# Optimization experiments

Hardware: AMD Instinct MI355X
Metric: run time of the kernel (lower is better)

## Reference

```python
import jax, jax.numpy as jnp
import numpy as np

IMG = 640
NUM_CLASSES = 80
B = 8
MAX_BOXES = 32
ALPHA, GAMMA = 0.25, 2.0
EPS = 1e-7


def make_anchors(img_size=IMG):
    strides = [8, 16, 32, 64, 128]
    scales = [2.0 ** 0, 2.0 ** (1.0 / 3.0), 2.0 ** (2.0 / 3.0)]
    ratios = [0.5, 1.0, 2.0]
    out = []
    for s in strides:
        base = 4.0 * s
        fs = img_size // s
        cs = (np.arange(fs) + 0.5) * s
        cy, cx = np.meshgrid(cs, cs, indexing='ij')
        for r in ratios:
            for sc in scales:
                w = base * sc / np.sqrt(r)
                h = base * sc * np.sqrt(r)
                a = np.stack([cx - w / 2, cy - h / 2, cx + w / 2, cy + h / 2], axis=-1).reshape(-1, 4)
                out.append(a)
    return np.concatenate(out, 0).astype(np.float32)  # [76725, 4]


def setup_inputs() -> dict:
    key = jax.random.key(0)
    k1, k2 = jax.random.split(key)
    anchors = jnp.asarray(make_anchors())
    Na = anchors.shape[0]
    cls_pred = jax.random.uniform(k1, (B, NUM_CLASSES, Na), dtype=jnp.float32)
    reg_pred = jax.random.normal(k2, (B, 4, Na), dtype=jnp.float32)
    rng = np.random.RandomState(0)
    x1 = rng.uniform(0, 500, (B, MAX_BOXES)).astype(np.float32)
    y1 = rng.uniform(0, 500, (B, MAX_BOXES)).astype(np.float32)
    w = rng.uniform(10, 140, (B, MAX_BOXES)).astype(np.float32)
    h = rng.uniform(10, 140, (B, MAX_BOXES)).astype(np.float32)
    cls = rng.randint(0, NUM_CLASSES, (B, MAX_BOXES)).astype(np.float32)
    nb = rng.randint(0, MAX_BOXES + 1, (B,))
    pad = np.arange(MAX_BOXES)[None, :] >= nb[:, None]
    cls[pad] = -1.0
    annots = jnp.asarray(np.stack([x1, y1, x1 + w, y1 + h, cls], axis=-1))  # [B,32,5]
    return {"cls_pred": cls_pred, "reg_pred": reg_pred, "annots": annots, "anchors": anchors}


def calc_iou(anchors, boxes):
    # anchors [Na,4], boxes [Nb,4] -> [Na,Nb]
    a_area = ((anchors[:, 2] - anchors[:, 0]) * (anchors[:, 3] - anchors[:, 1]))[:, None]
    b_area = (boxes[:, 2] - boxes[:, 0]) * (boxes[:, 3] - boxes[:, 1])
    iw = jnp.clip(jnp.minimum(anchors[:, 2:3], boxes[:, 2]) - jnp.maximum(anchors[:, 0:1], boxes[:, 0]), 0.0)
    ih = jnp.clip(jnp.minimum(anchors[:, 3:4], boxes[:, 3]) - jnp.maximum(anchors[:, 1:2], boxes[:, 1]), 0.0)
    inter = iw * ih
    union = jnp.clip(a_area + b_area - inter, 1e-7)
    return inter / union


def multibox_loss(cls_pred, reg_pred, annots, anchors):
    aw = anchors[:, 2] - anchors[:, 0]
    ah = anchors[:, 3] - anchors[:, 1]
    acx = anchors[:, 0] + 0.5 * aw
    acy = anchors[:, 1] + 0.5 * ah
    p = jnp.clip(cls_pred, EPS, 1.0 - EPS)
    C = cls_pred.shape[1]

    def per_image(classification, regression, annot):
        valid = annot[:, 4] != -1.0  # [Nb]
        iou = jnp.where(valid[None, :], calc_iou(anchors, annot[:, :4]), -1.0)  # [Na,Nb]
        iou_max = iou.max(axis=1)
        iou_arg = iou.argmax(axis=1)
        positive = iou_max >= 0.5  # [Na]
        num_pos = positive.sum().astype(jnp.float32)
        assigned = annot[iou_arg]  # [Na,5]
        tgt_cls = jnp.where(positive, assigned[:, 4].astype(jnp.int32), -1)
        targets = jax.nn.one_hot(tgt_cls, C, dtype=classification.dtype).T  # [C,Na]
        # focal loss (alpha=0.25, gamma=2) on clamped probabilities
        bce = -(targets * jnp.log(classification) + (1.0 - targets) * jnp.log1p(-classification))
        pt = targets * classification + (1.0 - targets) * (1.0 - classification)
        alpha_t = ALPHA * targets + (1.0 - ALPHA) * (1.0 - targets)
        cls_loss = (alpha_t * (1.0 - pt) ** GAMMA * bce).sum() / jnp.maximum(num_pos, 1.0)
        gw_raw = assigned[:, 2] - assigned[:, 0]
        gh_raw = assigned[:, 3] - assigned[:, 1]
        gcx = assigned[:, 0] + 0.5 * gw_raw
        gcy = assigned[:, 1] + 0.5 * gh_raw
        gw = jnp.clip(gw_raw, 1.0)
        gh = jnp.clip(gh_raw, 1.0)
        dx = (gcx - acx) / aw / 0.1
        dy = (gcy - acy) / ah / 0.1
        dw = jnp.log(gw / aw) / 0.2
        dh = jnp.log(gh / ah) / 0.2
        t = jnp.stack((dx, dy, dw, dh))  # [4,Na]
        diff = jnp.abs(t - regression)
        sl1 = jnp.where(diff <= 1.0 / 9.0, 0.5 * 9.0 * diff * diff, diff - 0.5 / 9.0)
        posf = positive.astype(regression.dtype)[None, :]
        reg_loss = jnp.where(num_pos > 0, (sl1 * posf).sum() / jnp.maximum(4.0 * num_pos, 1.0), 0.0)
        return cls_loss, reg_loss

    cls_l, reg_l = jax.vmap(per_image)(p, reg_pred, annots)
    return cls_l.mean() + reg_l.mean()


def reference(cls_pred, reg_pred, annots, anchors):
    return multibox_loss(cls_pred, reg_pred, annots, anchors)
```

## Files before the change

### kernel.cpp

```cpp
#include <hip/hip_runtime.h>
#include <math.h>


namespace {

constexpr int C  = 80;
constexpr int MB = 32;

__device__ __forceinline__ float clampp(float p) {
    return __builtin_amdgcn_fmed3f(p, 1e-7f, (float)(1.0 - 1e-7));
}

__global__ __launch_bounds__(256) void assign_kernel(
    const float* __restrict__ cls_pred,
    const float* __restrict__ reg_pred,
    const float* __restrict__ annots,
    const float* __restrict__ anchors,
    double* __restrict__ cls_sum,
    double* __restrict__ reg_sum,
    unsigned int* __restrict__ num_pos,
    int Na)
{
    const int b   = blockIdx.y;
    const int tid = threadIdx.x;
    const int a   = blockIdx.x * 256 + tid;
    const bool inb = (a < Na);

    __shared__ float4 sbox[MB];
    __shared__ float2 smeta[MB];
    __shared__ double swd[4];
    __shared__ float  swf[4];
    __shared__ int    swi[4];

    if (tid < MB) {
        const float* an = annots + ((size_t)b * MB + tid) * 5;
        float x1 = an[0], y1 = an[1], x2 = an[2], y2 = an[3];
        const float cl = an[4];
        if (cl == -1.0f) { x1 = y1 = x2 = y2 = -1e30f; }
        sbox[tid]  = make_float4(x1, y1, x2, y2);
        smeta[tid] = make_float2(__fmul_rn(__fsub_rn(x2, x1), __fsub_rn(y2, y1)), cl);
    }
    __syncthreads();

    float ax1 = 0.f, ay1 = 0.f, ax2 = 0.f, ay2 = 0.f;
    if (inb) {
        const float4 av = *reinterpret_cast<const float4*>(anchors + (size_t)a * 4);
        ax1 = av.x; ay1 = av.y; ax2 = av.z; ay2 = av.w;
    }
    const float a_area = __fmul_rn(__fsub_rn(ax2, ax1), __fsub_rn(ay2, ay1));

    float ibest = -1.0f, ubest = 1.0f;
    int   jbest = 0;
    #pragma unroll
    for (int j = 0; j < MB; ++j) {
        const float4 bx = sbox[j];
        const float2 bm = smeta[j];
        const float iw    = fmaxf(__fsub_rn(fminf(ax2, bx.z), fmaxf(ax1, bx.x)), 0.0f);
        const float ih    = fmaxf(__fsub_rn(fminf(ay2, bx.w), fmaxf(ay1, bx.y)), 0.0f);
        const float inter = __fmul_rn(iw, ih);
        const float uni   = fmaxf(__fsub_rn(__fadd_rn(a_area, bm.x), inter), 1e-7f);
        if (inter * ubest > ibest * uni) { ibest = inter; ubest = uni; jbest = j; }
    }

    double corr   = 0.0;
    float  my_reg = 0.0f;
    int    my_pos = 0;
    if (inb && __fdiv_rn(ibest, ubest) >= 0.5f) {
        my_pos = 1;
        const float4 g  = sbox[jbest];
        const int    tc = (int)smeta[jbest].y;

        const float aw  = ax2 - ax1,          ah  = ay2 - ay1;
        const float acx = ax1 + 0.5f * aw,    acy = ay1 + 0.5f * ah;
        const float gwr = g.z - g.x,          ghr = g.w - g.y;
        const float gcx = g.x + 0.5f * gwr,   gcy = g.y + 0.5f * ghr;
        const float gw  = fmaxf(gwr, 1.0f),   gh  = fmaxf(ghr, 1.0f);
        float t[4];
        t[0] = ((gcx - acx) / aw) / 0.1f;
        t[1] = ((gcy - acy) / ah) / 0.1f;
        t[2] = __logf(gw / aw) / 0.2f;
        t[3] = __logf(gh / ah) / 0.2f;
        const size_t rb = ((size_t)b * 4) * (size_t)Na + (size_t)a;
        #pragma unroll
        for (int k = 0; k < 4; ++k) {
            const float d = fabsf(t[k] - reg_pred[rb + (size_t)k * Na]);
            my_reg += (d <= (1.0f / 9.0f)) ? 4.5f * d * d : d - (0.5f / 9.0f);
        }

        float p = clampp(cls_pred[((size_t)b * C + tc) * (size_t)Na + (size_t)a]);
        const float om = __fsub_rn(1.0f, p);
        const float q  = __fsub_rn(1.0f, om);
        const float Ln = __logf(om);
        const float Lp = __logf(p);
        const float neg = -0.75f * __fmul_rn(__fmul_rn(q, q), Ln);
        const float pos = 0.25f * __fmul_rn(__fmul_rn(om, om), -Lp);
        corr = (double)pos - (double)neg;
    }

    double rc = corr;
    float  rr = my_reg;
    int    rp = my_pos;
    #pragma unroll
    for (int off = 32; off > 0; off >>= 1) {
        rc += __shfl_down(rc, off);
        rr += __shfl_down(rr, off);
        rp += __shfl_down(rp, off);
    }
    const int w = tid >> 6;
    if ((tid & 63) == 0) { swd[w] = rc; swf[w] = rr; swi[w] = rp; }
    __syncthreads();
    if (tid == 0) {
        double tcorr = 0.0; float treg = 0.f; int tpos = 0;
        #pragma unroll
        for (int i = 0; i < 4; ++i) { tcorr += swd[i]; treg += swf[i]; tpos += swi[i]; }
        if (tcorr != 0.0) atomicAdd(&cls_sum[b], tcorr);
        if (treg  != 0.f) atomicAdd(&reg_sum[b], (double)treg);
        if (tpos)         atomicAdd(&num_pos[b], (unsigned int)tpos);
    }
}

__global__ __launch_bounds__(256) void negsum_kernel(
    const float* __restrict__ cls_pred,
    double* __restrict__ cls_sum,
    int Na)
{
    const int b = blockIdx.y;
    const float4* __restrict__ base =
        reinterpret_cast<const float4*>(cls_pred + (size_t)b * C * (size_t)Na);
    const int n4     = (C * Na) >> 2;
    const int stride = gridDim.x * 256;

    float a0 = 0.f, a1 = 0.f, a2 = 0.f, a3 = 0.f;
    #pragma unroll 4
    for (int i = blockIdx.x * 256 + threadIdx.x; i < n4; i += stride) {
        const float4 v = base[i];
        {   const float p = clampp(v.x);
            const float om = __fsub_rn(1.0f, p);
            const float q  = __fsub_rn(1.0f, om);
            a0 = fmaf(__fmul_rn(__fmul_rn(q, q), __logf(om)), -0.75f, a0); }
        {   const float p = clampp(v.y);
            const float om = __fsub_rn(1.0f, p);
            const float q  = __fsub_rn(1.0f, om);
            a1 = fmaf(__fmul_rn(__fmul_rn(q, q), __logf(om)), -0.75f, a1); }
        {   const float p = clampp(v.z);
            const float om = __fsub_rn(1.0f, p);
            const float q  = __fsub_rn(1.0f, om);
            a2 = fmaf(__fmul_rn(__fmul_rn(q, q), __logf(om)), -0.75f, a2); }
        {   const float p = clampp(v.w);
            const float om = __fsub_rn(1.0f, p);
            const float q  = __fsub_rn(1.0f, om);
            a3 = fmaf(__fmul_rn(__fmul_rn(q, q), __logf(om)), -0.75f, a3); }
    }
    float csum = (a0 + a1) + (a2 + a3);

    #pragma unroll
    for (int off = 32; off > 0; off >>= 1) csum += __shfl_down(csum, off);
    __shared__ float sw[4];
    const int tid = threadIdx.x;
    const int w = tid >> 6;
    if ((tid & 63) == 0) sw[w] = csum;
    __syncthreads();
    if (tid == 0) {
        const float tot = (sw[0] + sw[1]) + (sw[2] + sw[3]);
        atomicAdd(&cls_sum[b], (double)tot);
    }
}

__global__ void finalize_kernel(const double* __restrict__ cls_sum,
                                const double* __restrict__ reg_sum,
                                const unsigned int* __restrict__ num_pos,
                                float* __restrict__ out, int B)
{
    if (threadIdx.x == 0 && blockIdx.x == 0) {
        double tot = 0.0;
        for (int b = 0; b < B; ++b) {
            const double np = (double)num_pos[b];
            tot += cls_sum[b] / fmax(np, 1.0);
            if (np > 0.0) tot += reg_sum[b] / (4.0 * np);
        }
        out[0] = (float)(tot / (double)B);
    }
}

}

extern "C" void kernel_launch(void* const* d_in, const int* in_sizes, int n_in,
                              void* d_out, int out_size, void* d_ws, size_t ws_size,
                              hipStream_t stream)
{
    const float* cls_pred = (const float*)d_in[0];
    const float* reg_pred = (const float*)d_in[1];
    const float* annots   = (const float*)d_in[2];
    const float* anchors  = (const float*)d_in[3];
    float* out = (float*)d_out;

    const int Na = in_sizes[3] / 4;
    const int B  = in_sizes[2] / (MB * 5);

    double*       cls_sum = (double*)d_ws;
    double*       reg_sum = cls_sum + B;
    unsigned int* num_pos = (unsigned int*)(reg_sum + B);

    hipMemsetAsync(d_ws, 0,
                   (size_t)(2 * B) * sizeof(double) + (size_t)B * sizeof(unsigned int),
                   stream);

    dim3 grid1((Na + 255) / 256, B);
    assign_kernel<<<grid1, 256, 0, stream>>>(cls_pred, reg_pred, annots, anchors,
                                             cls_sum, reg_sum, num_pos, Na);

    dim3 grid2(256, B);
    negsum_kernel<<<grid2, 256, 0, stream>>>(cls_pred, cls_sum, Na);

    finalize_kernel<<<1, 64, 0, stream>>>(cls_sum, reg_sum, num_pos, out, B);
}
```

Baseline: 294.0 us.

## Fuse assign and negative-sum kernels into one launch with per-block partials

Merges the anchor-assignment kernel and the negative focal-sum kernel into a single launch, split by block index range. Global double atomics and the workspace memset are replaced by per-block partial-sum buffers, which a 64-thread finalize kernel reduces with wave shuffles. This removes one kernel launch, the memset and atomic contention, and lets the two independent workloads run concurrently on the GPU. In exchange, the finalize kernel now reads more partial values, and block scheduling mixes two workloads with different costs.

```diff
diff --git a/kernel.cpp b/kernel.cpp
--- a/kernel.cpp
+++ b/kernel.cpp
@@ -4,33 +4,70 @@
 
 namespace {
 
-constexpr int C  = 80;
-constexpr int MB = 32;
+constexpr int C      = 80;
+constexpr int MB     = 32;
+constexpr int NB_NEG = 256;
 
 __device__ __forceinline__ float clampp(float p) {
     return __builtin_amdgcn_fmed3f(p, 1e-7f, (float)(1.0 - 1e-7));
 }
 
-__global__ __launch_bounds__(256) void assign_kernel(
+__device__ __forceinline__ float neg_term(float pin) {
+    const float p  = clampp(pin);
+    const float om = __fsub_rn(1.0f, p);
+    const float q  = __fsub_rn(1.0f, om);
+    return -0.75f * __fmul_rn(__fmul_rn(q, q), __logf(om));
+}
+
+__global__ __launch_bounds__(256) void main_kernel(
     const float* __restrict__ cls_pred,
     const float* __restrict__ reg_pred,
     const float* __restrict__ annots,
     const float* __restrict__ anchors,
-    double* __restrict__ cls_sum,
-    double* __restrict__ reg_sum,
-    unsigned int* __restrict__ num_pos,
-    int Na)
+    double* __restrict__ negPart,
+    double* __restrict__ corrPart,
+    float*  __restrict__ regPart,
+    int*    __restrict__ posPart,
+    int Na, int nbA)
 {
     const int b   = blockIdx.y;
     const int tid = threadIdx.x;
-    const int a   = blockIdx.x * 256 + tid;
-    const bool inb = (a < Na);
 
     __shared__ float4 sbox[MB];
     __shared__ float2 smeta[MB];
     __shared__ double swd[4];
     __shared__ float  swf[4];
     __shared__ int    swi[4];
+
+    if (blockIdx.x < NB_NEG) {
+        const float4* __restrict__ base =
+            reinterpret_cast<const float4*>(cls_pred + (size_t)b * C * (size_t)Na);
+        const int n4     = (C * Na) >> 2;
+        const int stride = NB_NEG * 256;
+
+        float a0 = 0.f, a1 = 0.f, a2 = 0.f, a3 = 0.f;
+        #pragma unroll 4
+        for (int i = blockIdx.x * 256 + tid; i < n4; i += stride) {
+            const float4 v = base[i];
+            a0 += neg_term(v.x);
+            a1 += neg_term(v.y);
+            a2 += neg_term(v.z);
+            a3 += neg_term(v.w);
+        }
+        float csum = (a0 + a1) + (a2 + a3);
+        #pragma unroll
+        for (int off = 32; off > 0; off >>= 1) csum += __shfl_down(csum, off);
+        if ((tid & 63) == 0) swf[tid >> 6] = csum;
+        __syncthreads();
+        if (tid == 0)
+            negPart[(size_t)b * NB_NEG + blockIdx.x] =
+                (double)((swf[0] + swf[1]) + (swf[2] + swf[3]));
+        return;
+    }
+
+    const int bx  = blockIdx.x - NB_NEG;
+    const int a   = bx * 256 + tid;
+    const bool inb = (a < Na);
 
     if (tid < MB) {
         const float* an = annots + ((size_t)b * MB + tid) * 5;
@@ -53,10 +90,10 @@
     int   jbest = 0;
     #pragma unroll
     for (int j = 0; j < MB; ++j) {
-        const float4 bx = sbox[j];
-        const float2 bm = smeta[j];
-        const float iw    = fmaxf(__fsub_rn(fminf(ax2, bx.z), fmaxf(ax1, bx.x)), 0.0f);
-        const float ih    = fmaxf(__fsub_rn(fminf(ay2, bx.w), fmaxf(ay1, bx.y)), 0.0f);
+        const float4 bxv = sbox[j];
+        const float2 bm  = smeta[j];
+        const float iw    = fmaxf(__fsub_rn(fminf(ax2, bxv.z), fmaxf(ax1, bxv.x)), 0.0f);
+        const float ih    = fmaxf(__fsub_rn(fminf(ay2, bxv.w), fmaxf(ay1, bxv.y)), 0.0f);
         const float inter = __fmul_rn(iw, ih);
         const float uni   = fmaxf(__fsub_rn(__fadd_rn(a_area, bm.x), inter), 1e-7f);
         if (inter * ubest > ibest * uni) { ibest = inter; ubest = uni; jbest = j; }
@@ -87,14 +124,10 @@
             my_reg += (d <= (1.0f / 9.0f)) ? 4.5f * d * d : d - (0.5f / 9.0f);
         }
 
-        float p = clampp(cls_pred[((size_t)b * C + tc) * (size_t)Na + (size_t)a]);
+        const float p  = clampp(cls_pred[((size_t)b * C + tc) * (size_t)Na + (size_t)a]);
         const float om = __fsub_rn(1.0f, p);
-        const float q  = __fsub_rn(1.0f, om);
-        const float Ln = __logf(om);
-        const float Lp = __logf(p);
-        const float neg = -0.75f * __fmul_rn(__fmul_rn(q, q), Ln);
-        const float pos = 0.25f * __fmul_rn(__fmul_rn(om, om), -Lp);
-        corr = (double)pos - (double)neg;
+        const float pos = 0.25f * __fmul_rn(__fmul_rn(om, om), -__logf(p));
+        corr = (double)pos - (double)neg_term(p);
     }
 
     double rc = corr;
@@ -113,73 +146,44 @@
         double tcorr = 0.0; float treg = 0.f; int tpos = 0;
         #pragma unroll
         for (int i = 0; i < 4; ++i) { tcorr += swd[i]; treg += swf[i]; tpos += swi[i]; }
-        if (tcorr != 0.0) atomicAdd(&cls_sum[b], tcorr);
-        if (treg  != 0.f) atomicAdd(&reg_sum[b], (double)treg);
-        if (tpos)         atomicAdd(&num_pos[b], (unsigned int)tpos);
-    }
-}
-
-__global__ __launch_bounds__(256) void negsum_kernel(
-    const float* __restrict__ cls_pred,
-    double* __restrict__ cls_sum,
-    int Na)
+        const size_t s = (size_t)b * nbA + bx;
+        corrPart[s] = tcorr;
+        regPart[s]  = treg;
+        posPart[s]  = tpos;
+    }
+}
+
+__global__ void finalize_kernel(const double* __restrict__ negPart,
+                                const double* __restrict__ corrPart,
+                                const float*  __restrict__ regPart,
+                                const int*    __restrict__ posPart,
+                                float* __restrict__ out, int B, int nbA)
 {
-    const int b = blockIdx.y;
-    const float4* __restrict__ base =
-        reinterpret_cast<const float4*>(cls_pred + (size_t)b * C * (size_t)Na);
-    const int n4     = (C * Na) >> 2;
-    const int stride = gridDim.x * 256;
-
-    float a0 = 0.f, a1 = 0.f, a2 = 0.f, a3 = 0.f;
-    #pragma unroll 4
-    for (int i = blockIdx.x * 256 + threadIdx.x; i < n4; i += stride) {
-        const float4 v = base[i];
-        {   const float p = clampp(v.x);
-            const float om = __fsub_rn(1.0f, p);
-            const float q  = __fsub_rn(1.0f, om);
-            a0 = fmaf(__fmul_rn(__fmul_rn(q, q), __logf(om)), -0.75f, a0); }
-        {   const float p = clampp(v.y);
-            const float om = __fsub_rn(1.0f, p);
-            const float q  = __fsub_rn(1.0f, om);
-            a1 = fmaf(__fmul_rn(__fmul_rn(q, q), __logf(om)), -0.75f, a1); }
-        {   const float p = clampp(v.z);
-            const float om = __fsub_rn(1.0f, p);
-            const float q  = __fsub_rn(1.0f, om);
-            a2 = fmaf(__fmul_rn(__fmul_rn(q, q), __logf(om)), -0.75f, a2); }
-        {   const float p = clampp(v.w);
-            const float om = __fsub_rn(1.0f, p);
-            const float q  = __fsub_rn(1.0f, om);
-            a3 = fmaf(__fmul_rn(__fmul_rn(q, q), __logf(om)), -0.75f, a3); }
-    }
-    float csum = (a0 + a1) + (a2 + a3);
-
-    #pragma unroll
-    for (int off = 32; off > 0; off >>= 1) csum += __shfl_down(csum, off);
-    __shared__ float sw[4];
     const int tid = threadIdx.x;
-    const int w = tid >> 6;
-    if ((tid & 63) == 0) sw[w] = csum;
-    __syncthreads();
-    if (tid == 0) {
-        const float tot = (sw[0] + sw[1]) + (sw[2] + sw[3]);
-        atomicAdd(&cls_sum[b], (double)tot);
-    }
-}
-
-__global__ void finalize_kernel(const double* __restrict__ cls_sum,
-                                const double* __restrict__ reg_sum,
-                                const unsigned int* __restrict__ num_pos,
-                                float* __restrict__ out, int B)
-{
-    if (threadIdx.x == 0 && blockIdx.x == 0) {
-        double tot = 0.0;
-        for (int b = 0; b < B; ++b) {
-            const double np = (double)num_pos[b];
-            tot += cls_sum[b] / fmax(np, 1.0);
-            if (np > 0.0) tot += reg_sum[b] / (4.0 * np);
-        }
-        out[0] = (float)(tot / (double)B);
-    }
+    double tot = 0.0;
+    for (int b = 0; b < B; ++b) {
+        double cls = 0.0, reg = 0.0;
+        int    pos = 0;
+        for (int i = tid; i < NB_NEG; i += 64)
+            cls += negPart[(size_t)b * NB_NEG + i];
+        for (int i = tid; i < nbA; i += 64) {
+            cls += corrPart[(size_t)b * nbA + i];
+            reg += (double)regPart[(size_t)b * nbA + i];
+            pos += posPart[(size_t)b * nbA + i];
+        }
+        #pragma unroll
+        for (int off = 32; off > 0; off >>= 1) {
+            cls += __shfl_down(cls, off);
+            reg += __shfl_down(reg, off);
+            pos += __shfl_down(pos, off);
+        }
+        if (tid == 0) {
+            const double np = (double)pos;
+            tot += cls / fmax(np, 1.0);
+            if (np > 0.0) tot += reg / (4.0 * np);
+        }
+    }
+    if (tid == 0) out[0] = (float)(tot / (double)B);
 }
 
 }
@@ -194,23 +198,19 @@
     const float* anchors  = (const float*)d_in[3];
     float* out = (float*)d_out;
 
-    const int Na = in_sizes[3] / 4;
-    const int B  = in_sizes[2] / (MB * 5);
-
-    double*       cls_sum = (double*)d_ws;
-    double*       reg_sum = cls_sum + B;
-    unsigned int* num_pos = (unsigned int*)(reg_sum + B);
-
-    hipMemsetAsync(d_ws, 0,
-                   (size_t)(2 * B) * sizeof(double) + (size_t)B * sizeof(unsigned int),
-                   stream);
-
-    dim3 grid1((Na + 255) / 256, B);
-    assign_kernel<<<grid1, 256, 0, stream>>>(cls_pred, reg_pred, annots, anchors,
-                                             cls_sum, reg_sum, num_pos, Na);
-
-    dim3 grid2(256, B);
-    negsum_kernel<<<grid2, 256, 0, stream>>>(cls_pred, cls_sum, Na);
-
-    finalize_kernel<<<1, 64, 0, stream>>>(cls_sum, reg_sum, num_pos, out, B);
-}
+    const int Na  = in_sizes[3] / 4;
+    const int B   = in_sizes[2] / (MB * 5);
+    const int nbA = (Na + 255) / 256;
+
+    double* negPart  = (double*)d_ws;
+    double* corrPart = negPart + (size_t)B * NB_NEG;
+    float*  regPart  = (float*)(corrPart + (size_t)B * nbA);
+    int*    posPart  = (int*)(regPart + (size_t)B * nbA);
+
+    dim3 grid(NB_NEG + nbA, B);
+    main_kernel<<<grid, 256, 0, stream>>>(cls_pred, reg_pred, annots, anchors,
+                                          negPart, corrPart, regPart, posPart,
+                                          Na, nbA);
+    finalize_kernel<<<1, 64, 0, stream>>>(negPart, corrPart, regPart, posPart,
+                                          out, B, nbA);
+}
```

Result: no change. 294.5 us (+0.2%).
